# Performance work log

Hardware: AMD Instinct MI355X
Metric: run time of the kernel (lower is better)

## Reference

```python
import jax, jax.numpy as jnp
import numpy as np

B, S, D, H, F = 64, 256, 512, 8, 2048
NB = 2
L = NB + 2 * NB  # blocks_1 (NB) + blocks_2 (2*NB) = 6 attention layers
DH = D // H
FC1, FC2 = 512, 256  # final_fc_dim, final_fc_dim // 2


def setup_inputs() -> dict:
    key = jax.random.key(0)
    ks = jax.random.split(key, 32)
    w = lambda k, shape, s: jax.random.normal(k, shape, dtype=jnp.float32) * s
    sD = D ** -0.5
    return {
        "q_embed_data": w(ks[0], (B, S, D), 1.0),
        "qa_embed_data": w(ks[1], (B, S, D), 1.0),
        "Wq": w(ks[2], (L, D, D), sD), "bq": jnp.zeros((L, D), jnp.float32),
        "Wk": w(ks[3], (L, D, D), sD), "bk": jnp.zeros((L, D), jnp.float32),
        "Wv": w(ks[4], (L, D, D), sD), "bv": jnp.zeros((L, D), jnp.float32),
        "Wo": w(ks[5], (L, D, D), sD), "bo": jnp.zeros((L, D), jnp.float32),
        "gammas": w(ks[6], (L, H), 1.0),
        "ln1_g": jnp.ones((L, D), jnp.float32), "ln1_b": jnp.zeros((L, D), jnp.float32),
        "W1": w(ks[7], (L, D, F), sD), "b1": jnp.zeros((L, F), jnp.float32),
        "W2": w(ks[8], (L, F, D), F ** -0.5), "b2": jnp.zeros((L, D), jnp.float32),
        "ln2_g": jnp.ones((L, D), jnp.float32), "ln2_b": jnp.zeros((L, D), jnp.float32),
        "O1": w(ks[9], (2 * D, FC1), (2 * D) ** -0.5), "bO1": jnp.zeros((FC1,), jnp.float32),
        "O2": w(ks[10], (FC1, FC2), FC1 ** -0.5), "bO2": jnp.zeros((FC2,), jnp.float32),
        "O3": w(ks[11], (FC2, 1), FC2 ** -0.5), "bO3": jnp.zeros((1,), jnp.float32),
    }


def _layer_norm(x, g, b):
    mu = x.mean(-1, keepdims=True)
    var = ((x - mu) ** 2).mean(-1, keepdims=True)
    return (x - mu) * jax.lax.rsqrt(var + 1e-5) * g + b


def _akt_attention(q, k, v, mask, gamma, zero_pad):
    # q,k,v: [B,H,S,DH]; mask: [S,S] bool; gamma: [H]
    neg = jnp.float32(-1e32)
    scores = jnp.einsum('bhqd,bhkd->bhqk', q, k) / np.sqrt(DH).astype(np.float32)
    # monotonic distance-decay (detached in the original): softmax'd scores -> cumulative distance
    sm = jax.nn.softmax(jnp.where(mask, scores, neg), axis=-1) * mask
    sm = jax.lax.stop_gradient(sm)
    distcum = jnp.cumsum(sm, axis=-1)
    disttot = jnp.sum(sm, axis=-1, keepdims=True)
    idx = jnp.arange(S)
    pos = jnp.abs(idx[:, None] - idx[None, :]).astype(jnp.float32)  # |x1 - x2|
    dist = jnp.sqrt(jnp.clip((disttot - distcum) * pos, 0.0, None))
    g = -jax.nn.softplus(gamma)[None, :, None, None]
    total_effect = jnp.clip(jnp.exp(dist * g), 1e-5, 1e5)
    scores = jnp.where(mask, scores * total_effect, neg)
    attn = jax.nn.softmax(scores, axis=-1)
    if zero_pad:
        attn = attn.at[:, :, 0, :].set(0.0)  # zero first query row
    out = jnp.einsum('bhqk,bhkd->bhqd', attn, v)
    return out, attn


def reference(q_embed_data, qa_embed_data, Wq, bq, Wk, bk, Wv, bv, Wo, bo, gammas,
              ln1_g, ln1_b, W1, b1, W2, b2, ln2_g, ln2_b, O1, bO1, O2, bO2, O3, bO3):
    idx = jnp.arange(S)
    mask_incl = idx[:, None] >= idx[None, :]  # mask==1: current + past
    mask_excl = idx[:, None] > idx[None, :]   # mask==0: strictly past

    def block(i, query, key_, vals, incl, zero_pad, apply_pos):
        proj = lambda x, W, b: (x @ W + b).reshape(B, S, H, DH).transpose(0, 2, 1, 3)
        qh, kh, vh = proj(query, Wq[i], bq[i]), proj(key_, Wk[i], bk[i]), proj(vals, Wv[i], bv[i])
        o, attn = _akt_attention(qh, kh, vh, mask_incl if incl else mask_excl, gammas[i], zero_pad)
        o = o.transpose(0, 2, 1, 3).reshape(B, S, D) @ Wo[i] + bo[i]
        q2 = _layer_norm(query + o, ln1_g[i], ln1_b[i])
        if apply_pos:
            h = jax.nn.relu(q2 @ W1[i] + b1[i]) @ W2[i] + b2[i]
            q2 = _layer_norm(q2 + h, ln2_g[i], ln2_b[i])
        return q2, attn

    y = qa_embed_data
    x = q_embed_data
    li = 0
    for _ in range(NB):  # blocks_1: knowledge encoder, self-attn, mask=1
        y, _ = block(li, y, y, y, incl=True, zero_pad=False, apply_pos=True)
        li += 1
    attn = None
    flag_first = True
    for _ in range(2 * NB):  # blocks_2: alternating question self-attn / knowledge retriever
        if flag_first:
            x, _ = block(li, x, x, x, incl=True, zero_pad=False, apply_pos=False)
            flag_first = False
        else:
            x, attn = block(li, x, x, y, incl=False, zero_pad=True, apply_pos=True)
            flag_first = True
        li += 1

    concat_q = jnp.concatenate([x, q_embed_data], axis=-1)  # [B,S,2D]
    h = jax.nn.relu(concat_q @ O1 + bO1)
    h = jax.nn.relu(h @ O2 + bO2)
    preds = jax.nn.sigmoid((h @ O3 + bO3)[..., 0])  # [B,S]
    return preds
```

## Files before the change

kernel.cpp:

```cpp
#include <hip/hip_runtime.h>

typedef unsigned short u16;
typedef unsigned int u32;
typedef short short8 __attribute__((ext_vector_type(8)));
typedef float f32x4 __attribute__((ext_vector_type(4)));

#define DEV static __device__ __forceinline__

DEV u16 f2bf(float f) {
  u32 u = __builtin_bit_cast(u32, f);
  u32 r = u + 0x7FFFu + ((u >> 16) & 1u);
  return (u16)(r >> 16);
}
DEV float bf2f(u16 h) { u32 u = ((u32)h) << 16; return __builtin_bit_cast(float, u); }

DEV u32 cvtpk(float lo, float hi_) {
  u32 r;
  asm("v_cvt_pk_bf16_f32 %0, %1, %2" : "=v"(r) : "v"(lo), "v"(hi_));
  return r;
}

DEV void async16(const u16* g, u16* l) {
  __builtin_amdgcn_global_load_lds((const __attribute__((address_space(1))) void*)g,
                                   (__attribute__((address_space(3))) void*)l, 16, 0, 0);
}

template<bool RELU, bool OUTBF, bool RESID, bool SPLIT3>
__global__ __launch_bounds__(256, 2) void gemm_kernel(
    const u16* __restrict__ A, const u16* __restrict__ A2, int KA,
    int lda, int lda2,
    const u16* __restrict__ Bt, int K,
    const float* __restrict__ bias, const float* __restrict__ resid,
    float* __restrict__ Cf, u16* __restrict__ Cb, u16* __restrict__ Cb2, u16* __restrict__ Cb3,
    int ldc)
{
  __shared__ u16 smem[2][16384];
  const int tid = threadIdx.x, wave = tid >> 6, lane = tid & 63;
  const int m0 = blockIdx.x * 128, n0 = blockIdx.y * 128;
  const int wr = wave >> 1, wc = wave & 1;
  const int lj = lane & 15, hi = lane >> 4;

  f32x4 acc[4][4];
  const f32x4 zz = {0.f, 0.f, 0.f, 0.f};
#pragma unroll
  for (int i = 0; i < 4; i++)
#pragma unroll
    for (int j = 0; j < 4; j++) acc[i][j] = zz;

  const int nkt = K / 64;

  auto stage = [&](int buf, int kt) {
    int kofs = kt * 64;
    const u16* sa; int la;
    if (kofs < KA) { sa = A + kofs; la = lda; }
    else           { sa = A2 + (kofs - KA); la = lda2; }
#pragma unroll
    for (int i = 0; i < 8; i++) {
      int c = wave * 8 + i;
      if (c < 16) {
        const u16* g = sa + (size_t)(m0 + c * 8 + (lane >> 3)) * la + (lane & 7) * 8;
        async16(g, &smem[buf][c * 512]);
      } else {
        const u16* g = Bt + (size_t)(n0 + (c - 16) * 8 + (lane >> 3)) * K + kofs + (lane & 7) * 8;
        async16(g, &smem[buf][c * 512]);
      }
    }
  };

  stage(0, 0);
  int cur = 0;
  for (int kt = 0; kt < nkt; kt++) {
    __syncthreads();
    if (kt + 1 < nkt) stage(cur ^ 1, kt + 1);
    const u16* la_ = &smem[cur][0];
    const u16* lb_ = &smem[cur][8192];
#pragma unroll
    for (int ks = 0; ks < 2; ks++) {
      short8 af[4], bfr[4];
#pragma unroll
      for (int mi = 0; mi < 4; mi++)
        af[mi] = *(const short8*)(la_ + (wr * 64 + mi * 16 + lj) * 64 + ks * 32 + hi * 8);
#pragma unroll
      for (int ni = 0; ni < 4; ni++)
        bfr[ni] = *(const short8*)(lb_ + (wc * 64 + ni * 16 + lj) * 64 + ks * 32 + hi * 8);
#pragma unroll
      for (int mi = 0; mi < 4; mi++)
#pragma unroll
        for (int ni = 0; ni < 4; ni++)
          acc[mi][ni] = __builtin_amdgcn_mfma_f32_16x16x32_bf16(af[mi], bfr[ni], acc[mi][ni], 0, 0, 0);
    }
    cur ^= 1;
  }

  u16* outB = Cb;
  int nloc = n0;
  if (SPLIT3) {
    int sec = n0 >> 9;
    outB = (sec == 0) ? Cb : (sec == 1) ? Cb2 : Cb3;
    nloc = n0 & 511;
  }

  float bv[4];
#pragma unroll
  for (int ni = 0; ni < 4; ni++) bv[ni] = bias[n0 + wc * 64 + ni * 16 + lj];
#pragma unroll
  for (int mi = 0; mi < 4; mi++)
#pragma unroll
    for (int r = 0; r < 4; r++) {
      int row = m0 + wr * 64 + mi * 16 + hi * 4 + r;
      size_t rb = (size_t)row * ldc;
#pragma unroll
      for (int ni = 0; ni < 4; ni++) {
        int col = nloc + wc * 64 + ni * 16 + lj;
        float v = acc[mi][ni][r] + bv[ni];
        if (RESID) v += resid[rb + col];
        if (RELU) v = fmaxf(v, 0.f);
        if (OUTBF) outB[rb + col] = f2bf(v);
        else Cf[rb + col] = v;
      }
    }
}

template<bool RELU, bool SPLIT3>
__global__ __launch_bounds__(512) void gemm256_kernel(
    const u16* __restrict__ A, const u16* __restrict__ A2v, int lda,
    const u16* __restrict__ Bt, int K,
    const float* __restrict__ bias,
    u16* __restrict__ Cb, u16* __restrict__ Cb2, u16* __restrict__ Cb3, int ldc)
{
  __shared__ u16 smem[65536];
  const int tid = threadIdx.x, wave = tid >> 6, lane = tid & 63;
  const int m0 = blockIdx.x * 256, n0 = blockIdx.y * 256;
  const int wm = wave >> 2, wn = wave & 3;
  const int lj = lane & 15, hi = lane >> 4;
  const int srow = wave * 8 + (lane >> 3);
  const int schunk = (lane & 7) ^ ((lane >> 3) & 7);

  const u16* Asrc = (SPLIT3 && (n0 >> 9) == 2 && A2v) ? A2v : A;

  f32x4 acc[8][4];
  const f32x4 zz = {0.f, 0.f, 0.f, 0.f};
#pragma unroll
  for (int i = 0; i < 8; i++)
#pragma unroll
    for (int j = 0; j < 4; j++) acc[i][j] = zz;

  const int nkt = K / 64;

  auto stageA = [&](int buf, int kt, int seg) {
    const u16* g = Asrc + (size_t)(m0 + seg * 64 + srow) * lda + kt * 64 + schunk * 8;
    async16(g, &smem[buf * 16384 + (seg * 64 + wave * 8) * 64]);
  };
  auto stageB = [&](int buf, int kt, int seg) {
    const u16* g = Bt + (size_t)(n0 + seg * 64 + srow) * K + kt * 64 + schunk * 8;
    async16(g, &smem[32768 + buf * 16384 + (seg * 64 + wave * 8) * 64]);
  };

#pragma unroll
  for (int seg = 0; seg < 4; seg++) stageA(0, 0, seg);
#pragma unroll
  for (int seg = 0; seg < 4; seg++) stageB(0, 0, seg);

  int cur = 0;
  for (int t = 0; t < nkt; t++) {
    const bool pf = (t + 1 < nkt);
    const char* aB = (const char*)smem + cur * 32768;
    const char* bB = (const char*)smem + 65536 + cur * 32768;
#pragma unroll
    for (int ph = 0; ph < 4; ph++) {
      const int mh = ph >> 1, nh = ph & 1;
      if (pf) {
        if (ph < 2) { stageA(cur ^ 1, t + 1, ph * 2); stageA(cur ^ 1, t + 1, ph * 2 + 1); }
        else        { stageB(cur ^ 1, t + 1, (ph - 2) * 2); stageB(cur ^ 1, t + 1, (ph - 2) * 2 + 1); }
      }
      if (ph == 0) {
        if (pf) asm volatile("s_waitcnt vmcnt(2)" ::: "memory");
        else    asm volatile("s_waitcnt vmcnt(0)" ::: "memory");
      }
      __builtin_amdgcn_s_barrier();

      short8 af[4][2], bfr[2][2];
#pragma unroll
      for (int mi = 0; mi < 4; mi++) {
        int row = wm * 128 + (mh * 4 + mi) * 16 + lj;
#pragma unroll
        for (int ks = 0; ks < 2; ks++)
          af[mi][ks] = *(const short8*)(aB + row * 128 + ((ks * 64 + hi * 16) ^ ((row & 7) << 4)));
      }
#pragma unroll
      for (int ni = 0; ni < 2; ni++) {
        int row = wn * 64 + (nh * 2 + ni) * 16 + lj;
#pragma unroll
        for (int ks = 0; ks < 2; ks++)
          bfr[ni][ks] = *(const short8*)(bB + row * 128 + ((ks * 64 + hi * 16) ^ ((row & 7) << 4)));
      }
      __builtin_amdgcn_s_setprio(1);
#pragma unroll
      for (int mi = 0; mi < 4; mi++)
#pragma unroll
        for (int ni = 0; ni < 2; ni++)
#pragma unroll
          for (int ks = 0; ks < 2; ks++)
            acc[mh * 4 + mi][nh * 2 + ni] =
                __builtin_amdgcn_mfma_f32_16x16x32_bf16(af[mi][ks], bfr[ni][ks],
                                                        acc[mh * 4 + mi][nh * 2 + ni], 0, 0, 0);
      __builtin_amdgcn_s_setprio(0);
      __builtin_amdgcn_s_barrier();
    }
    cur ^= 1;
  }

  u16* outB = Cb;
  int nloc = n0;
  if (SPLIT3) {
    int sec = n0 >> 9;
    outB = (sec == 0) ? Cb : (sec == 1) ? Cb2 : Cb3;
    nloc = n0 & 511;
  }

  float bv[4];
#pragma unroll
  for (int ni = 0; ni < 4; ni++) bv[ni] = bias[n0 + wn * 64 + ni * 16 + lj];
#pragma unroll
  for (int mi = 0; mi < 8; mi++)
#pragma unroll
    for (int r = 0; r < 4; r++) {
      int row = m0 + wm * 128 + mi * 16 + hi * 4 + r;
      size_t rb = (size_t)row * ldc;
#pragma unroll
      for (int ni = 0; ni < 4; ni++) {
        int col = nloc + wn * 64 + ni * 16 + lj;
        float v = acc[mi][ni][r] + bv[ni];
        if (RELU) v = fmaxf(v, 0.f);
        outB[rb + col] = f2bf(v);
      }
    }
}

__global__ __launch_bounds__(512) void gemmln_kernel(
    const u16* __restrict__ A, int lda,
    const u16* __restrict__ Bt, int K,
    const float* __restrict__ bias, const float* __restrict__ resid,
    const float* __restrict__ gamma, const float* __restrict__ beta,
    float* __restrict__ outF, u16* __restrict__ outB)
{
  __shared__ u16 smem[73728];
  const int tid = threadIdx.x, wave = tid >> 6, lane = tid & 63;
  const int m0 = blockIdx.x * 64;
  const int lj = lane & 15, hi = lane >> 4;
  const int srow = lane >> 3;
  const int schunk = (lane & 7) ^ ((lane >> 3) & 7);

  f32x4 acc[4][4];
  const f32x4 zz = {0.f, 0.f, 0.f, 0.f};
#pragma unroll
  for (int i = 0; i < 4; i++)
#pragma unroll
    for (int j = 0; j < 4; j++) acc[i][j] = zz;

  const int nkt = K / 64;

  auto stageA = [&](int buf, int kt) {
    const u16* g = A + (size_t)(m0 + wave * 8 + srow) * lda + kt * 64 + schunk * 8;
    async16(g, &smem[buf * 4096 + (wave * 8) * 64]);
  };
  auto stageB = [&](int buf, int kt, int seg) {
    const u16* g = Bt + (size_t)(seg * 64 + wave * 8 + srow) * K + kt * 64 + schunk * 8;
    async16(g, &smem[8192 + buf * 32768 + (seg * 64 + wave * 8) * 64]);
  };

  stageA(0, 0);
#pragma unroll
  for (int seg = 0; seg < 8; seg++) stageB(0, 0, seg);

  int cur = 0;
  for (int t = 0; t < nkt; t++) {
    const bool pf = (t + 1 < nkt);
    if (pf) {
      stageA(cur ^ 1, t + 1);
#pragma unroll
      for (int seg = 0; seg < 8; seg++) stageB(cur ^ 1, t + 1, seg);
    }
    if (pf) asm volatile("s_waitcnt vmcnt(9)" ::: "memory");
    else    asm volatile("s_waitcnt vmcnt(0)" ::: "memory");
    __builtin_amdgcn_s_barrier();

    const char* aB = (const char*)smem + cur * 8192;
    const char* bB = (const char*)smem + 16384 + cur * 65536;
    short8 af[4][2], bfr[4][2];
#pragma unroll
    for (int mi = 0; mi < 4; mi++) {
      int row = mi * 16 + lj;
#pragma unroll
      for (int ks = 0; ks < 2; ks++)
        af[mi][ks] = *(const short8*)(aB + row * 128 + ((ks * 64 + hi * 16) ^ ((row & 7) << 4)));
    }
#pragma unroll
    for (int ni = 0; ni < 4; ni++) {
      int row = wave * 64 + ni * 16 + lj;
#pragma unroll
      for (int ks = 0; ks < 2; ks++)
        bfr[ni][ks] = *(const short8*)(bB + row * 128 + ((ks * 64 + hi * 16) ^ ((row & 7) << 4)));
    }
    __builtin_amdgcn_s_setprio(1);
#pragma unroll
    for (int mi = 0; mi < 4; mi++)
#pragma unroll
      for (int ni = 0; ni < 4; ni++)
#pragma unroll
        for (int ks = 0; ks < 2; ks++)
          acc[mi][ni] = __builtin_amdgcn_mfma_f32_16x16x32_bf16(af[mi][ks], bfr[ni][ks],
                                                                acc[mi][ni], 0, 0, 0);
    __builtin_amdgcn_s_setprio(0);
    __builtin_amdgcn_s_barrier();
    cur ^= 1;
  }

  float bv[4], gv[4], btv[4];
  int col[4];
#pragma unroll
  for (int ni = 0; ni < 4; ni++) {
    col[ni] = wave * 64 + ni * 16 + lj;
    bv[ni] = bias[col[ni]];
    gv[ni] = gamma[col[ni]];
    btv[ni] = beta[col[ni]];
  }

  float* red = (float*)smem;

#pragma unroll
  for (int mi = 0; mi < 4; mi++)
#pragma unroll
    for (int r = 0; r < 4; r++) {
      int lrow = mi * 16 + hi * 4 + r;
      size_t rb = (size_t)(m0 + lrow) * 512;
      float s = 0.f, q = 0.f;
#pragma unroll
      for (int ni = 0; ni < 4; ni++) {
        float v = acc[mi][ni][r] + bv[ni] + resid[rb + col[ni]];
        acc[mi][ni][r] = v;
        s += v; q += v * v;
      }
#pragma unroll
      for (int m = 1; m <= 8; m <<= 1) { s += __shfl_xor(s, m); q += __shfl_xor(q, m); }
      if (lj == 0) { red[lrow * 16 + wave * 2] = s; red[lrow * 16 + wave * 2 + 1] = q; }
    }
  __syncthreads();

#pragma unroll
  for (int mi = 0; mi < 4; mi++)
#pragma unroll
    for (int r = 0; r < 4; r++) {
      int lrow = mi * 16 + hi * 4 + r;
      size_t rb = (size_t)(m0 + lrow) * 512;
      float s = 0.f, q = 0.f;
#pragma unroll
      for (int w = 0; w < 8; w++) { s += red[lrow * 16 + w * 2]; q += red[lrow * 16 + w * 2 + 1]; }
      float mu = s * (1.f / 512.f);
      float var = q * (1.f / 512.f) - mu * mu;
      float rs = rsqrtf(fmaxf(var, 0.f) + 1e-5f);
#pragma unroll
      for (int ni = 0; ni < 4; ni++) {
        float y = (acc[mi][ni][r] - mu) * rs * gv[ni] + btv[ni];
        outF[rb + col[ni]] = y;
        outB[rb + col[ni]] = f2bf(y);
      }
    }
}

template<bool INCL, bool ZP>
__global__ __launch_bounds__(512) void attn_kernel(
    const u16* __restrict__ qb, const u16* __restrict__ kb, const u16* __restrict__ vb,
    u16* __restrict__ ob, const float* __restrict__ gammas, int li)
{
  __shared__ u16 smem[32768];
  const int tid = threadIdx.x, wave = tid >> 6, lane = tid & 63;
  const int h = blockIdx.x, b = blockIdx.y;
  const int lj = lane & 15, hi = lane >> 4;
  const size_t rowbase = (size_t)b * 256 * 512 + h * 64;

#pragma unroll
  for (int p = 0; p < 2; p++) {
    int r2 = p * 128 + (tid >> 3) * 2;
    int cc = (tid & 7) * 8;
    union { uint4 v; u16 e[8]; } v0, v1;
    uint4 k0 = *(const uint4*)(kb + rowbase + (size_t)r2 * 512 + cc);
    uint4 k1 = *(const uint4*)(kb + rowbase + (size_t)(r2 + 1) * 512 + cc);
    v0.v = *(const uint4*)(vb + rowbase + (size_t)r2 * 512 + cc);
    v1.v = *(const uint4*)(vb + rowbase + (size_t)(r2 + 1) * 512 + cc);
    *(uint4*)((char*)smem + r2 * 128 + ((cc * 2) ^ ((r2 & 7) << 4))) = k0;
    *(uint4*)((char*)smem + (r2 + 1) * 128 + ((cc * 2) ^ (((r2 + 1) & 7) << 4))) = k1;
#pragma unroll
    for (int i = 0; i < 8; i++) {
      int d = cc + i;
      u32 pk = (u32)v0.e[i] | ((u32)v1.e[i] << 16);
      *(u32*)((char*)smem + 32768 + d * 512 + ((2 * r2) ^ ((d & 7) << 4))) = pk;
    }
  }

  const int qt0 = wave, qt1 = 15 - wave;

  short8 qfa[2][2];
#pragma unroll
  for (int cf = 0; cf < 2; cf++) {
    int t = cf ? qt1 : qt0;
#pragma unroll
    for (int s = 0; s < 2; s++)
      qfa[cf][s] = *(const short8*)(qb + rowbase + (size_t)(t * 16 + lj) * 512 + s * 32 + hi * 8);
  }

  float gm = gammas[li * 8 + h];
  float geff = -(gm > 20.f ? gm : log1pf(__expf(gm)));

  __syncthreads();

  const f32x4 zz = {0.f, 0.f, 0.f, 0.f};
  const int hsel = hi >> 1;
  const int sbase = lj + 32 * (hi & 1);

#pragma unroll
  for (int cf = 0; cf < 2; cf++) {
    const int t = cf ? qt1 : qt0;
    const int qb0 = t * 16;
    const int q = qb0 + lj;
    const int nrf = t + 1;
    const int nsp = (t + 2) >> 1;

    f32x4 acc[16], E[16];
#pragma unroll
    for (int rf = 0; rf < 16; rf++) acc[rf] = zz;

#pragma unroll
    for (int rf = 0; rf < 16; rf++) {
      if (rf >= nrf) continue;
      int row = rf * 16 + lj;
#pragma unroll
      for (int s = 0; s < 2; s++) {
        short8 kf = *(const short8*)((char*)smem + row * 128 + ((s * 64 + hi * 16) ^ ((row & 7) << 4)));
        acc[rf] = __builtin_amdgcn_mfma_f32_16x16x32_bf16(kf, qfa[cf][s], acc[rf], 0, 0, 0);
      }
    }

    float mx = -1e30f;
#pragma unroll
    for (int rf = 0; rf < 16; rf++) {
      if (rf >= nrf) continue;
#pragma unroll
      for (int r = 0; r < 4; r++) {
        acc[rf][r] *= 0.125f;
        int k = rf * 16 + hi * 4 + r;
        bool valid = INCL ? (k <= q) : (k < q);
        mx = fmaxf(mx, valid ? acc[rf][r] : -1e30f);
      }
    }
    mx = fmaxf(mx, __shfl_xor(mx, 16));
    mx = fmaxf(mx, __shfl_xor(mx, 32));
    float sum = 0.f;
#pragma unroll
    for (int rf = 0; rf < 16; rf++) {
      if (rf >= nrf) continue;
#pragma unroll
      for (int r = 0; r < 4; r++) {
        int k = rf * 16 + hi * 4 + r;
        bool valid = INCL ? (k <= q) : (k < q);
        float ev = valid ? __expf(acc[rf][r] - mx) : 0.f;
        E[rf][r] = ev;
        sum += ev;
      }
    }
    sum += __shfl_xor(sum, 16);
    sum += __shfl_xor(sum, 32);
    float inv1 = sum > 0.f ? 1.f / sum : 0.f;
    float dtot = sum > 0.f ? 1.f : 0.f;

    float run = 0.f;
#pragma unroll
    for (int rf = 0; rf < 16; rf++) {
      if (rf >= nrf) continue;
      float p[4];
      float pa = 0.f;
#pragma unroll
      for (int r = 0; r < 4; r++) {
        pa += E[rf][r] * inv1;
        p[r] = pa;
      }
      float tl = p[3];
      float v = tl;
      float u1 = __shfl_up(v, 16); v += (hi >= 1) ? u1 : 0.f;
      float u2 = __shfl_up(v, 32); v += (hi >= 2) ? u2 : 0.f;
      float T = __shfl(v, lj + 48);
      float cbase = run + (v - tl);
#pragma unroll
      for (int r = 0; r < 4; r++) {
        int k = rf * 16 + hi * 4 + r;
        bool valid = INCL ? (k <= q) : (k < q);
        float tail = fmaxf(dtot - (cbase + p[r]), 0.f);
        float pos = (float)(q - k);
        float dist = sqrtf(tail * pos);
        float te = fmaxf(__expf(dist * geff), 1e-5f);
        acc[rf][r] = valid ? acc[rf][r] * te : -1e32f;
      }
      run += T;
    }

    float mx2 = -3.0e38f;
#pragma unroll
    for (int rf = 0; rf < 16; rf++) {
      if (rf >= nrf) continue;
#pragma unroll
      for (int r = 0; r < 4; r++) mx2 = fmaxf(mx2, acc[rf][r]);
    }
    mx2 = fmaxf(mx2, __shfl_xor(mx2, 16));
    mx2 = fmaxf(mx2, __shfl_xor(mx2, 32));
    float sum2 = 0.f;
#pragma unroll
    for (int rf = 0; rf < 16; rf++) {
      if (rf >= nrf) continue;
#pragma unroll
      for (int r = 0; r < 4; r++) {
        float ev = __expf(acc[rf][r] - mx2);
        acc[rf][r] = ev;
        sum2 += ev;
      }
    }
    sum2 += __shfl_xor(sum2, 16);
    sum2 += __shfl_xor(sum2, 32);
    float inv = 1.f / sum2;
    if (ZP) { if (q == 0) inv = 0.f; }
#pragma unroll
    for (int rf = 0; rf < 16; rf++) {
      if (rf >= nrf) continue;
#pragma unroll
      for (int r = 0; r < 4; r++) acc[rf][r] *= inv;
    }

    f32x4 oacc[4];
#pragma unroll
    for (int j = 0; j < 4; j++) oacc[j] = zz;

#pragma unroll
    for (int sp = 0; sp < 8; sp++) {
      if (sp >= nsp) continue;
      u32 a0 = cvtpk(acc[2 * sp][0],     acc[2 * sp][1]);
      u32 a1 = cvtpk(acc[2 * sp][2],     acc[2 * sp][3]);
      u32 b0 = cvtpk(acc[2 * sp + 1][0], acc[2 * sp + 1][1]);
      u32 b1 = cvtpk(acc[2 * sp + 1][2], acc[2 * sp + 1][3]);
      u32 pw[4];
#pragma unroll
      for (int tt = 0; tt < 4; tt++) {
        int src = sbase + 16 * (tt >> 1);
        u32 za = (u32)__shfl((int)((tt & 1) ? a1 : a0), src);
        u32 zb = (u32)__shfl((int)((tt & 1) ? b1 : b0), src);
        pw[tt] = hsel ? zb : za;
      }
      short8 pf = __builtin_bit_cast(short8, *(uint4*)pw);
#pragma unroll
      for (int nf = 0; nf < 4; nf++) {
        int d = nf * 16 + lj;
        short8 vf = *(const short8*)((char*)smem + 32768 + d * 512 + ((sp * 64 + hi * 16) ^ ((d & 7) << 4)));
        oacc[nf] = __builtin_amdgcn_mfma_f32_16x16x32_bf16(pf, vf, oacc[nf], 0, 0, 0);
      }
    }

#pragma unroll
    for (int r = 0; r < 4; r++) {
      int qr = qb0 + hi * 4 + r;
      size_t obase = (size_t)(b * 256 + qr) * 512 + h * 64;
#pragma unroll
      for (int nf = 0; nf < 4; nf++)
        ob[obase + nf * 16 + lj] = f2bf(oacc[nf][r]);
    }
  }
}

__global__ void cvt_kernel(const float* __restrict__ in, u16* __restrict__ out, int n8)
{
  int i = blockIdx.x * 256 + threadIdx.x;
  if (i >= n8) return;
  float4 a = ((const float4*)in)[2 * i], c = ((const float4*)in)[2 * i + 1];
  union { uint4 v; u16 e[8]; } pk;
  pk.e[0]=f2bf(a.x); pk.e[1]=f2bf(a.y); pk.e[2]=f2bf(a.z); pk.e[3]=f2bf(a.w);
  pk.e[4]=f2bf(c.x); pk.e[5]=f2bf(c.y); pk.e[6]=f2bf(c.z); pk.e[7]=f2bf(c.w);
  ((uint4*)out)[i] = pk.v;
}

__global__ void trans_kernel(const float* __restrict__ in, u16* __restrict__ out,
                             int R, int C, size_t istr, size_t ostr)
{
  __shared__ float tile[32][33];
  in += (size_t)blockIdx.z * istr;
  out += (size_t)blockIdx.z * ostr;
  int c0 = blockIdx.x * 32, r0 = blockIdx.y * 32;
  int tx = threadIdx.x & 31, ty = threadIdx.x >> 5;
#pragma unroll
  for (int i = 0; i < 4; i++) tile[ty + i * 8][tx] = in[(size_t)(r0 + ty + i * 8) * C + c0 + tx];
  __syncthreads();
#pragma unroll
  for (int i = 0; i < 4; i++) out[(size_t)(c0 + ty + i * 8) * R + r0 + tx] = f2bf(tile[tx][ty + i * 8]);
}

__global__ void bias_concat_kernel(const float* __restrict__ bq, const float* __restrict__ bk,
                                   const float* __restrict__ bv, float* __restrict__ out)
{
  int t = blockIdx.x * 256 + threadIdx.x;
  if (t >= 6 * 1536) return;
  int li = t / 1536, c = t % 1536;
  float v = (c < 512) ? bq[li * 512 + c]
          : (c < 1024) ? bk[li * 512 + c - 512]
                       : bv[li * 512 + c - 1024];
  out[t] = v;
}

__global__ __launch_bounds__(256) void pred_kernel(const u16* __restrict__ h2,
    const float* __restrict__ O3, const float* __restrict__ bO3, float* __restrict__ out)
{
  int row = blockIdx.x * 4 + (threadIdx.x >> 6), lane = threadIdx.x & 63;
  union { uint2 v; u16 e[4]; } hv;
  hv.v = *(const uint2*)(h2 + (size_t)row * 256 + lane * 4);
  float d = 0.f;
#pragma unroll
  for (int i = 0; i < 4; i++) d += bf2f(hv.e[i]) * O3[lane * 4 + i];
#pragma unroll
  for (int m = 1; m <= 32; m <<= 1) d += __shfl_xor(d, m);
  if (lane == 0) out[row] = 1.f / (1.f + expf(-(d + bO3[0])));
}

extern "C" void kernel_launch(void* const* d_in, const int* in_sizes, int n_in,
                              void* d_out, int out_size, void* d_ws, size_t ws_size,
                              hipStream_t stream)
{
  const float* qe   = (const float*)d_in[0];
  const float* qa   = (const float*)d_in[1];
  const float* Wq   = (const float*)d_in[2];  const float* bq  = (const float*)d_in[3];
  const float* Wk   = (const float*)d_in[4];  const float* bk  = (const float*)d_in[5];
  const float* Wv   = (const float*)d_in[6];  const float* bv  = (const float*)d_in[7];
  const float* Wo   = (const float*)d_in[8];  const float* bo  = (const float*)d_in[9];
  const float* gam  = (const float*)d_in[10];
  const float* ln1g = (const float*)d_in[11]; const float* ln1b = (const float*)d_in[12];
  const float* W1   = (const float*)d_in[13]; const float* b1  = (const float*)d_in[14];
  const float* W2   = (const float*)d_in[15]; const float* b2  = (const float*)d_in[16];
  const float* ln2g = (const float*)d_in[17]; const float* ln2b = (const float*)d_in[18];
  const float* O1   = (const float*)d_in[19]; const float* bO1 = (const float*)d_in[20];
  const float* O2   = (const float*)d_in[21]; const float* bO2 = (const float*)d_in[22];
  const float* O3   = (const float*)d_in[23]; const float* bO3 = (const float*)d_in[24];
  float* preds = (float*)d_out;

  const int M = 16384;
  const int BIG = 0x3fffffff;
  char* ws = (char*)d_ws;
  size_t off = 0;
  auto alloc = [&](size_t bytes) { char* p = ws + off; off += (bytes + 255) & ~(size_t)255; return p; };

  u16* wqkvt = (u16*)alloc((size_t)6*1536*512*2);
  u16* wot   = (u16*)alloc((size_t)6*512*512*2);
  u16* w1t   = (u16*)alloc((size_t)6*2048*512*2);
  u16* w2t   = (u16*)alloc((size_t)6*512*2048*2);
  u16* o1t   = (u16*)alloc((size_t)512*1024*2);
  u16* o2t   = (u16*)alloc((size_t)256*512*2);
  float* bqkv = (float*)alloc((size_t)6*1536*4);
  u16* qx  = (u16*)alloc((size_t)M*512*2);
  u16* sA  = (u16*)alloc((size_t)M*512*2);
  u16* sB  = (u16*)alloc((size_t)M*512*2);
  float* g1 = (float*)alloc((size_t)M*512*4);
  u16* region = (u16*)alloc((size_t)M*2048*2);
  u16* qbf = region;
  u16* kbf = region + (size_t)M*512;
  u16* vbf = region + (size_t)2*M*512;
  u16* obf = region + (size_t)3*M*512;
  u16* h1  = region;
  u16* hd1 = region;
  u16* hd2 = region + (size_t)2*M*512;
  (void)ws_size; (void)in_sizes; (void)n_in; (void)out_size;

  trans_kernel<<<dim3(16, 16, 6), 256, 0, stream>>>(Wq, wqkvt,                          512, 512,  (size_t)512*512,  (size_t)1536*512);
  trans_kernel<<<dim3(16, 16, 6), 256, 0, stream>>>(Wk, wqkvt + (size_t)512*512,        512, 512,  (size_t)512*512,  (size_t)1536*512);
  trans_kernel<<<dim3(16, 16, 6), 256, 0, stream>>>(Wv, wqkvt + (size_t)1024*512,       512, 512,  (size_t)512*512,  (size_t)1536*512);
  trans_kernel<<<dim3(16, 16, 6), 256, 0, stream>>>(Wo, wot,                            512, 512,  (size_t)512*512,  (size_t)512*512);
  trans_kernel<<<dim3(64, 16, 6), 256, 0, stream>>>(W1, w1t,                            512, 2048, (size_t)512*2048, (size_t)2048*512);
  trans_kernel<<<dim3(16, 64, 6), 256, 0, stream>>>(W2, w2t,                            2048, 512, (size_t)2048*512, (size_t)512*2048);
  trans_kernel<<<dim3(16, 32, 1), 256, 0, stream>>>(O1, o1t,                            1024, 512, 0, 0);
  trans_kernel<<<dim3(8, 16, 1),  256, 0, stream>>>(O2, o2t,                            512, 256,  0, 0);
  bias_concat_kernel<<<36, 256, 0, stream>>>(bq, bk, bv, bqkv);
  cvt_kernel<<<4096, 256, 0, stream>>>(qe, qx, M * 512 / 8);
  cvt_kernel<<<4096, 256, 0, stream>>>(qa, sA, M * 512 / 8);

  const u16* curB = sA;
  const float* curF = qa;
  const u16* yfin = nullptr;
  const dim3 gA(8, 64);

  for (int li = 0; li < 6; li++) {
    bool ffn  = (li == 0 || li == 1 || li == 3 || li == 5);
    bool excl = (li == 3 || li == 5);
    size_t wqkv_off = (size_t)li * 1536 * 512;

    gemm256_kernel<false, true><<<dim3(64, 6), 512, 0, stream>>>(
        curB, excl ? yfin : curB, 512, wqkvt + wqkv_off, 512, bqkv + li * 1536,
        qbf, kbf, vbf, 512);

    if (!excl) attn_kernel<true,  false><<<gA, 512, 0, stream>>>(qbf, kbf, vbf, obf, gam, li);
    else       attn_kernel<false, true ><<<gA, 512, 0, stream>>>(qbf, kbf, vbf, obf, gam, li);

    gemmln_kernel<<<256, 512, 0, stream>>>(
        obf, 512, wot + (size_t)li * 512 * 512, 512, bo + li * 512,
        curF, ln1g + li * 512, ln1b + li * 512, g1, sB);
    curB = sB; curF = g1;

    if (ffn) {
      gemm256_kernel<true, false><<<dim3(64, 8), 512, 0, stream>>>(
          curB, nullptr, 512, w1t + (size_t)li * 2048 * 512, 512, b1 + li * 2048,
          h1, nullptr, nullptr, 2048);
      u16* nB = (li < 2) ? sA : sB;
      gemmln_kernel<<<256, 512, 0, stream>>>(
          h1, 2048, w2t + (size_t)li * 512 * 2048, 2048, b2 + li * 512,
          g1, ln2g + li * 512, ln2b + li * 512, g1, nB);
      curB = nB;
    }
    if (li == 1) { yfin = curB; curB = qx; curF = qe; }
  }

  gemm_kernel<true, true, false, false><<<dim3(128, 4), 256, 0, stream>>>(
      curB, qx, 512, 512, 512, o1t, 1024, bO1, nullptr, nullptr, hd1, nullptr, nullptr, 512);
  gemm_kernel<true, true, false, false><<<dim3(128, 2), 256, 0, stream>>>(
      hd1, hd1, BIG, 512, 512, o2t, 512, bO2, nullptr, nullptr, hd2, nullptr, nullptr, 256);
  pred_kernel<<<4096, 256, 0, stream>>>(hd2, O3, bO3, preds);
}
```

Measured before the change: 1.258 ms.

## Load GEMM-LN B operand directly into registers instead of staging through LDS

In the fused GEMM+LayerNorm kernel, each wave's B-operand fragments are now read straight from global memory into registers, double-buffered across two k-tiles. Only the A tile is still staged asynchronously into a much smaller LDS buffer. This removes the large LDS footprint and the LDS round trip for B, which should allow more resident blocks and fewer LDS reads. In exchange, the direct global loads are less coalesced, there are extra full barriers, and register pressure rises from holding two B fragment sets.

```diff
diff --git a/kernel.cpp b/kernel.cpp
--- a/kernel.cpp
+++ b/kernel.cpp
@@ -244,7 +244,7 @@
     const float* __restrict__ gamma, const float* __restrict__ beta,
     float* __restrict__ outF, u16* __restrict__ outB)
 {
-  __shared__ u16 smem[73728];
+  __shared__ u16 smem[2][4096];
   const int tid = threadIdx.x, wave = tid >> 6, lane = tid & 63;
   const int m0 = blockIdx.x * 64;
   const int lj = lane & 15, hi = lane >> 4;
@@ -262,32 +262,22 @@
 
   auto stageA = [&](int buf, int kt) {
     const u16* g = A + (size_t)(m0 + wave * 8 + srow) * lda + kt * 64 + schunk * 8;
-    async16(g, &smem[buf * 4096 + (wave * 8) * 64]);
+    async16(g, &smem[buf][(wave * 8) * 64]);
   };
-  auto stageB = [&](int buf, int kt, int seg) {
-    const u16* g = Bt + (size_t)(seg * 64 + wave * 8 + srow) * K + kt * 64 + schunk * 8;
-    async16(g, &smem[8192 + buf * 32768 + (seg * 64 + wave * 8) * 64]);
+
+  short8 bX[4][2], bY[4][2];
+  auto loadB = [&](short8 (&b)[4][2], int kt) {
+#pragma unroll
+    for (int ni = 0; ni < 4; ni++)
+#pragma unroll
+      for (int ks = 0; ks < 2; ks++)
+        b[ni][ks] = *(const short8*)(Bt + (size_t)(wave * 64 + ni * 16 + lj) * K
+                                     + kt * 64 + ks * 32 + hi * 8);
   };
 
-  stageA(0, 0);
-#pragma unroll
-  for (int seg = 0; seg < 8; seg++) stageB(0, 0, seg);
-
-  int cur = 0;
-  for (int t = 0; t < nkt; t++) {
-    const bool pf = (t + 1 < nkt);
-    if (pf) {
-      stageA(cur ^ 1, t + 1);
-#pragma unroll
-      for (int seg = 0; seg < 8; seg++) stageB(cur ^ 1, t + 1, seg);
-    }
-    if (pf) asm volatile("s_waitcnt vmcnt(9)" ::: "memory");
-    else    asm volatile("s_waitcnt vmcnt(0)" ::: "memory");
-    __builtin_amdgcn_s_barrier();
-
-    const char* aB = (const char*)smem + cur * 8192;
-    const char* bB = (const char*)smem + 16384 + cur * 65536;
-    short8 af[4][2], bfr[4][2];
+  auto compute = [&](int buf, short8 (&b)[4][2]) {
+    const char* aB = (const char*)smem[buf];
+    short8 af[4][2];
 #pragma unroll
     for (int mi = 0; mi < 4; mi++) {
       int row = mi * 16 + lj;
@@ -295,13 +285,6 @@
       for (int ks = 0; ks < 2; ks++)
         af[mi][ks] = *(const short8*)(aB + row * 128 + ((ks * 64 + hi * 16) ^ ((row & 7) << 4)));
     }
-#pragma unroll
-    for (int ni = 0; ni < 4; ni++) {
-      int row = wave * 64 + ni * 16 + lj;
-#pragma unroll
-      for (int ks = 0; ks < 2; ks++)
-        bfr[ni][ks] = *(const short8*)(bB + row * 128 + ((ks * 64 + hi * 16) ^ ((row & 7) << 4)));
-    }
     __builtin_amdgcn_s_setprio(1);
 #pragma unroll
     for (int mi = 0; mi < 4; mi++)
@@ -309,13 +292,24 @@
       for (int ni = 0; ni < 4; ni++)
 #pragma unroll
         for (int ks = 0; ks < 2; ks++)
-          acc[mi][ni] = __builtin_amdgcn_mfma_f32_16x16x32_bf16(af[mi][ks], bfr[ni][ks],
+          acc[mi][ni] = __builtin_amdgcn_mfma_f32_16x16x32_bf16(af[mi][ks], b[ni][ks],
                                                                 acc[mi][ni], 0, 0, 0);
     __builtin_amdgcn_s_setprio(0);
-    __builtin_amdgcn_s_barrier();
-    cur ^= 1;
-  }
-
+  };
+
+  stageA(0, 0);
+  loadB(bX, 0);
+
+  for (int t = 0; t < nkt; t += 2) {
+    __syncthreads();
+    if (t + 1 < nkt) { stageA(1, t + 1); loadB(bY, t + 1); }
+    compute(0, bX);
+    __syncthreads();
+    if (t + 2 < nkt) { stageA(0, t + 2); loadB(bX, t + 2); }
+    if (t + 1 < nkt) compute(1, bY);
+  }
+
+  __syncthreads();
   float bv[4], gv[4], btv[4];
   int col[4];
 #pragma unroll
```

After: 1.414 ms. 1.12x slower.
